# Kernel optimization log

Hardware: AMD Instinct MI355X
Metric: run time of the kernel (lower is better)

Reference implementation:

```python
import jax, jax.numpy as jnp
import numpy as np

DEGREE = 8
D = 512
K = 256
O = 512
N = 65536


def setup_inputs() -> dict:
    key = jax.random.key(0)
    ks = jax.random.split(key, 4)
    z = jax.random.normal(ks[0], (N, D), dtype=jnp.float32)
    T0 = jnp.ones((K,), dtype=jnp.float32)
    # T[i-1] corresponds to parameter T_i, i = 1..DEGREE, each [K, D]
    T = jax.random.normal(ks[1], (DEGREE, K, D), dtype=jnp.float32) * 0.02
    C_w = jax.random.normal(ks[2], (O, K), dtype=jnp.float32) * (1.0 / np.sqrt(K))
    C_b = jnp.zeros((O,), dtype=jnp.float32)
    return {"z": z, "T0": T0, "T": T, "C_w": C_w, "C_b": C_b}


def reference(z, T0, T, C_w, C_b):
    # z: [N, D]; T: [DEGREE, K, D]; recurrence over polynomial degree n:
    #   out_n = (z @ ((2n-1)/n * T_n).T) * out_{n-1} - (n-1)/n * out_{n-2}
    z = z.reshape(-1, D)
    out_prev2 = T0                                  # degree 0, [K] (broadcasts over N)
    out_prev1 = jnp.einsum('nd,kd->nk', z, T[0])    # degree 1, [N, K]
    for n in range(2, DEGREE + 1):
        a = (2.0 * n - 1.0) / n
        b = (n - 1.0) / n
        cur = jnp.einsum('nd,kd->nk', z, a * T[n - 1]) * out_prev1 - b * out_prev2
        out_prev2, out_prev1 = out_prev1, cur
    # layer_C applied to out_list[degree]
    return out_prev1 @ C_w.T + C_b
```

## Files before the change

kernel.cpp:

```cpp
#include <hip/hip_runtime.h>
#include <hip/hip_fp16.h>
#include <cstdint>

#define NROWS 65536
#define DIM   512
#define KDIM  256
#define ODIM  512
#define DEG   8
#define ZN    (NROWS * DIM)
#define TN    (DEG * KDIM * DIM)
#define CWN   (ODIM * KDIM)

typedef _Float16 f16x8 __attribute__((ext_vector_type(8)));
typedef float    f32x4 __attribute__((ext_vector_type(4)));


__device__ __forceinline__ void gld_lds16(const void* g, void* l) {
  __builtin_amdgcn_global_load_lds(
      (const __attribute__((address_space(1))) unsigned int*)g,
      (__attribute__((address_space(3))) unsigned int*)l, 16, 0, 0);
}

__device__ __forceinline__ unsigned pack2h(float a, float b) {
  union { _Float16 h[2]; unsigned u; } x;
  x.h[0] = (_Float16)a; x.h[1] = (_Float16)b;
  return x.u;
}

__device__ __forceinline__ int swz(int row, int chunk) {
  return (row << 7) | (((chunk + row) & 7) << 4);
}


__global__ void k_convert(const float* __restrict__ z,
                          const float* __restrict__ T,
                          const float* __restrict__ Cw,
                          _Float16* __restrict__ z16,
                          _Float16* __restrict__ Tb,
                          _Float16* __restrict__ Cwb) {
  long e = ((long)blockIdx.x * 256 + threadIdx.x) * 4;
  const float* src;
  _Float16* dst;
  float s = 1.0f;
  if (e < ZN) {
    src = z + e; dst = z16 + e;
  } else {
    long o = e - ZN;
    if (o < TN) {
      int n = (int)(o >> 17);
      s = (n == 0) ? 1.0f : (float)(2 * n + 1) / (float)(n + 1);
      src = T + o; dst = Tb + o;
    } else {
      long c = o - TN;
      if (c >= CWN) return;
      src = Cw + c; dst = Cwb + c;
    }
  }
  float4 v = *(const float4*)src;
  uint2 p; p.x = pack2h(v.x * s, v.y * s); p.y = pack2h(v.z * s, v.w * s);
  *(uint2*)dst = p;
}


__launch_bounds__(256, 3)
__global__ void k_poly(const _Float16* __restrict__ z16,
                       const float* __restrict__ T0,
                       const _Float16* __restrict__ Tb,
                       _Float16* __restrict__ u8) {
  __shared__ __align__(16) uint16_t As[128 * 64];
  __shared__ __align__(16) uint16_t Bs[2][128 * 64];

  const int tid = threadIdx.x;
  const int wave = tid >> 6, lane = tid & 63;

  const int id = blockIdx.x;
  const int super = id >> 8, rem = id & 255;
  const int kg = rem >> 4;
  const int rt = (super << 4) | (rem & 15);
  const int r0 = rt << 7;
  const int k0 = kg << 4;

  const int m_l = lane & 15, kq = lane >> 4;
  const int wrow = wave << 5;

  f32x4 acc[DEG][2];
#pragma unroll
  for (int n = 0; n < DEG; n++)
#pragma unroll
    for (int a = 0; a < 2; a++)
      acc[n][a] = (f32x4){0.f, 0.f, 0.f, 0.f};

  const _Float16* aptr[4];
  const _Float16* bptr[4];
  int lofs[4];
#pragma unroll
  for (int j = 0; j < 4; j++) {
    int lin = (j << 8) + tid;
    int row = lin >> 3;
    int c = ((lin & 7) - row) & 7;
    lofs[j] = lin << 4;
    aptr[j] = z16 + (size_t)(r0 + row) * DIM + (c << 3);
    int n = row >> 4, kk = row & 15;
    bptr[j] = Tb + (size_t)((n << 8) + k0 + kk) * DIM + (c << 3);
  }

#pragma unroll
  for (int j = 0; j < 4; j++) gld_lds16(bptr[j], (char*)Bs[0] + lofs[j]);
#pragma unroll
  for (int j = 0; j < 4; j++) bptr[j] += 64;

  for (int it = 0; it < DIM / 64; it++) {
    const int cur = it & 1;
    __builtin_amdgcn_sched_barrier(0);
    __builtin_amdgcn_s_barrier();
    __builtin_amdgcn_sched_barrier(0);

#pragma unroll
    for (int j = 0; j < 4; j++) gld_lds16(aptr[j], (char*)As + lofs[j]);
#pragma unroll
    for (int j = 0; j < 4; j++) aptr[j] += 64;

    if (it < DIM / 64 - 1) {
#pragma unroll
      for (int j = 0; j < 4; j++)
        gld_lds16(bptr[j], (char*)Bs[cur ^ 1] + lofs[j]);
#pragma unroll
      for (int j = 0; j < 4; j++) bptr[j] += 64;
      asm volatile("s_waitcnt vmcnt(4)" ::: "memory");
    } else {
      asm volatile("s_waitcnt vmcnt(0)" ::: "memory");
    }
    __builtin_amdgcn_sched_barrier(0);
    __builtin_amdgcn_s_barrier();
    __builtin_amdgcn_sched_barrier(0);

#pragma unroll
    for (int ks = 0; ks < 2; ks++) {
      const int chunk = (ks << 2) + kq;
      f16x8 af[2];
#pragma unroll
      for (int mf = 0; mf < 2; mf++)
        af[mf] = *(const f16x8*)((char*)As + swz(wrow + (mf << 4) + m_l, chunk));
#pragma unroll
      for (int n = 0; n < DEG; n++) {
        f16x8 bv = *(const f16x8*)((char*)Bs[cur] + swz((n << 4) + m_l, chunk));
#pragma unroll
        for (int mf = 0; mf < 2; mf++)
          acc[n][mf] = __builtin_amdgcn_mfma_f32_16x16x32_f16(
              af[mf], bv, acc[n][mf], 0, 0, 0);
      }
    }
  }

  const float bcoef[7] = {1.f/2.f, 2.f/3.f, 3.f/4.f, 4.f/5.f,
                          5.f/6.f, 6.f/7.f, 7.f/8.f};
  const int col = k0 + m_l;
  const float t0v = T0[col];
#pragma unroll
  for (int mf = 0; mf < 2; mf++) {
    f32x4 up2 = {t0v, t0v, t0v, t0v};
    f32x4 up1 = acc[0][mf];
#pragma unroll
    for (int n = 2; n <= DEG; n++) {
      f32x4 cur = acc[n - 1][mf] * up1 - bcoef[n - 2] * up2;
      up2 = up1; up1 = cur;
    }
    const int rbase = r0 + wrow + (mf << 4) + (kq << 2);
#pragma unroll
    for (int r = 0; r < 4; r++)
      u8[(size_t)(rbase + r) * KDIM + col] = (_Float16)up1[r];
  }
}


__launch_bounds__(256, 4)
__global__ void k_out(const _Float16* __restrict__ u8,
                      const _Float16* __restrict__ Cwb,
                      const float* __restrict__ Cb,
                      float* __restrict__ out) {
  __shared__ __align__(16) uint16_t As[2][128 * 64];
  __shared__ __align__(16) uint16_t Bs[64 * 64];

  const int tid = threadIdx.x;
  const int wave = tid >> 6, lane = tid & 63;

  const int id = blockIdx.x;
  const int xcd = id & 7;
  const int s = id >> 3;
  const int cg = s & 7;
  const int rt = (xcd << 6) | (s >> 3);
  const int r0 = rt << 7;
  const int c0 = cg << 6;

  const int m_l = lane & 15, kq = lane >> 4;
  const int wrow = wave << 5;

  f32x4 acc[2][4];
#pragma unroll
  for (int a = 0; a < 2; a++)
#pragma unroll
    for (int b = 0; b < 4; b++)
      acc[a][b] = (f32x4){0.f, 0.f, 0.f, 0.f};

  const _Float16* aptr[4];
  const _Float16* bptr[2];
  int lofsA[4], lofsB[2];
#pragma unroll
  for (int j = 0; j < 4; j++) {
    int lin = (j << 8) + tid;
    int row = lin >> 3;
    int c = ((lin & 7) - row) & 7;
    lofsA[j] = lin << 4;
    aptr[j] = u8 + (size_t)(r0 + row) * KDIM + (c << 3);
  }
#pragma unroll
  for (int j = 0; j < 2; j++) {
    int lin = (j << 8) + tid;
    int row = lin >> 3;
    int c = ((lin & 7) - row) & 7;
    lofsB[j] = lin << 4;
    bptr[j] = Cwb + (size_t)(c0 + row) * KDIM + (c << 3);
  }

#pragma unroll
  for (int j = 0; j < 4; j++) gld_lds16(aptr[j], (char*)As[0] + lofsA[j]);
#pragma unroll
  for (int j = 0; j < 4; j++) aptr[j] += 64;

  for (int it = 0; it < KDIM / 64; it++) {
    const int cur = it & 1;
    __builtin_amdgcn_sched_barrier(0);
    __builtin_amdgcn_s_barrier();
    __builtin_amdgcn_sched_barrier(0);

#pragma unroll
    for (int j = 0; j < 2; j++) gld_lds16(bptr[j], (char*)Bs + lofsB[j]);
#pragma unroll
    for (int j = 0; j < 2; j++) bptr[j] += 64;

    if (it < KDIM / 64 - 1) {
#pragma unroll
      for (int j = 0; j < 4; j++)
        gld_lds16(aptr[j], (char*)As[cur ^ 1] + lofsA[j]);
#pragma unroll
      for (int j = 0; j < 4; j++) aptr[j] += 64;
      asm volatile("s_waitcnt vmcnt(4)" ::: "memory");
    } else {
      asm volatile("s_waitcnt vmcnt(0)" ::: "memory");
    }
    __builtin_amdgcn_sched_barrier(0);
    __builtin_amdgcn_s_barrier();
    __builtin_amdgcn_sched_barrier(0);

#pragma unroll
    for (int ks = 0; ks < 2; ks++) {
      const int chunk = (ks << 2) + kq;
      f16x8 af[2];
#pragma unroll
      for (int mf = 0; mf < 2; mf++)
        af[mf] = *(const f16x8*)((char*)As[cur] + swz(wrow + (mf << 4) + m_l, chunk));
#pragma unroll
      for (int kf = 0; kf < 4; kf++) {
        f16x8 bv = *(const f16x8*)((char*)Bs + swz((kf << 4) + m_l, chunk));
#pragma unroll
        for (int mf = 0; mf < 2; mf++)
          acc[mf][kf] = __builtin_amdgcn_mfma_f32_16x16x32_f16(
              af[mf], bv, acc[mf][kf], 0, 0, 0);
      }
    }
  }

#pragma unroll
  for (int kf = 0; kf < 4; kf++) {
    const int col = c0 + (kf << 4) + m_l;
    const float cb = Cb[col];
#pragma unroll
    for (int mf = 0; mf < 2; mf++) {
      const int rbase = r0 + wrow + (mf << 4) + (kq << 2);
#pragma unroll
      for (int r = 0; r < 4; r++)
        out[(size_t)(rbase + r) * ODIM + col] = acc[mf][kf][r] + cb;
    }
  }
}


extern "C" void kernel_launch(void* const* d_in, const int* in_sizes, int n_in,
                              void* d_out, int out_size, void* d_ws, size_t ws_size,
                              hipStream_t stream) {
  const float* z  = (const float*)d_in[0];
  const float* T0 = (const float*)d_in[1];
  const float* T  = (const float*)d_in[2];
  const float* Cw = (const float*)d_in[3];
  const float* Cb = (const float*)d_in[4];
  float* out = (float*)d_out;

  char* ws = (char*)d_ws;
  _Float16* z16 = (_Float16*)ws;
  _Float16* Tb  = (_Float16*)(ws + (size_t)ZN * 2);
  _Float16* Cwb = (_Float16*)(ws + (size_t)ZN * 2 + (size_t)TN * 2);
  _Float16* u8  = (_Float16*)(ws + (size_t)ZN * 2 + (size_t)TN * 2 + (size_t)CWN * 2);

  k_convert<<<33920, 256, 0, stream>>>(z, T, Cw, z16, Tb, Cwb);
  k_poly<<<8192, 256, 0, stream>>>(z16, T0, Tb, u8);
  k_out<<<4096, 256, 0, stream>>>(u8, Cwb, Cb, out);
}
```

Baseline: 377.7 us.

## Register-prefetch A tiles in poly GEMM, double-buffer B in output GEMM, widen convert

The poly kernel now loads z tiles into registers two stages ahead and stores them to LDS itself, instead of issuing direct global-to-LDS loads that had to complete within the same iteration. This hides global latency behind the MFMA work. The output GEMM now double-buffers the C_w tile and prefetches both operands one stage ahead, lowering its occupancy hint from 4 to 3 blocks. The convert kernel handles 8 elements per thread with half the grid. The costs are extra registers and LDS, plus lower occupancy in k_out.

```diff
diff --git a/kernel.cpp b/kernel.cpp
--- a/kernel.cpp
+++ b/kernel.cpp
@@ -38,7 +38,7 @@
                           _Float16* __restrict__ z16,
                           _Float16* __restrict__ Tb,
                           _Float16* __restrict__ Cwb) {
-  long e = ((long)blockIdx.x * 256 + threadIdx.x) * 4;
+  long e = ((long)blockIdx.x * 256 + threadIdx.x) * 8;
   const float* src;
   _Float16* dst;
   float s = 1.0f;
@@ -56,9 +56,12 @@
       src = Cw + c; dst = Cwb + c;
     }
   }
-  float4 v = *(const float4*)src;
-  uint2 p; p.x = pack2h(v.x * s, v.y * s); p.y = pack2h(v.z * s, v.w * s);
-  *(uint2*)dst = p;
+  float4 v0 = *(const float4*)src;
+  float4 v1 = *(const float4*)(src + 4);
+  uint4 p;
+  p.x = pack2h(v0.x * s, v0.y * s); p.y = pack2h(v0.z * s, v0.w * s);
+  p.z = pack2h(v1.x * s, v1.y * s); p.w = pack2h(v1.z * s, v1.w * s);
+  *(uint4*)dst = p;
 }
 
 
@@ -104,32 +107,50 @@
     bptr[j] = Tb + (size_t)((n << 8) + k0 + kk) * DIM + (c << 3);
   }
 
+  uint4 aR[2][4];
+
+#pragma unroll
+  for (int j = 0; j < 4; j++)
+    aR[0][j] = *reinterpret_cast<const uint4*>(aptr[j]);
+  __builtin_amdgcn_sched_barrier(0);
 #pragma unroll
   for (int j = 0; j < 4; j++) gld_lds16(bptr[j], (char*)Bs[0] + lofs[j]);
-#pragma unroll
-  for (int j = 0; j < 4; j++) bptr[j] += 64;
-
+  __builtin_amdgcn_sched_barrier(0);
+#pragma unroll
+  for (int j = 0; j < 4; j++)
+    aR[1][j] = *reinterpret_cast<const uint4*>(aptr[j] + 64);
+  __builtin_amdgcn_sched_barrier(0);
+
+#pragma unroll
   for (int it = 0; it < DIM / 64; it++) {
     const int cur = it & 1;
-    __builtin_amdgcn_sched_barrier(0);
     __builtin_amdgcn_s_barrier();
-    __builtin_amdgcn_sched_barrier(0);
-
-#pragma unroll
-    for (int j = 0; j < 4; j++) gld_lds16(aptr[j], (char*)As + lofs[j]);
-#pragma unroll
-    for (int j = 0; j < 4; j++) aptr[j] += 64;
-
-    if (it < DIM / 64 - 1) {
+    if (it < DIM / 64 - 1)
+      asm volatile("s_waitcnt vmcnt(4)" ::: "memory");
+    else
+      asm volatile("s_waitcnt vmcnt(0)" ::: "memory");
+    __builtin_amdgcn_sched_barrier(0);
+
+#pragma unroll
+    for (int j = 0; j < 4; j++)
+      *(uint4*)((char*)As + lofs[j]) = aR[cur][j];
+    __builtin_amdgcn_sched_barrier(0);
+
+    if (it + 1 < DIM / 64) {
 #pragma unroll
       for (int j = 0; j < 4; j++)
-        gld_lds16(bptr[j], (char*)Bs[cur ^ 1] + lofs[j]);
-#pragma unroll
-      for (int j = 0; j < 4; j++) bptr[j] += 64;
-      asm volatile("s_waitcnt vmcnt(4)" ::: "memory");
-    } else {
-      asm volatile("s_waitcnt vmcnt(0)" ::: "memory");
-    }
+        gld_lds16(bptr[j] + ((it + 1) << 6), (char*)Bs[cur ^ 1] + lofs[j]);
+    }
+    __builtin_amdgcn_sched_barrier(0);
+
+    if (it + 2 < DIM / 64) {
+#pragma unroll
+      for (int j = 0; j < 4; j++)
+        aR[cur][j] = *reinterpret_cast<const uint4*>(aptr[j] + ((it + 2) << 6));
+    }
+    __builtin_amdgcn_sched_barrier(0);
+
+    asm volatile("s_waitcnt lgkmcnt(0)" ::: "memory");
     __builtin_amdgcn_sched_barrier(0);
     __builtin_amdgcn_s_barrier();
     __builtin_amdgcn_sched_barrier(0);
@@ -173,13 +194,13 @@
 }
 
 
-__launch_bounds__(256, 4)
+__launch_bounds__(256, 3)
 __global__ void k_out(const _Float16* __restrict__ u8,
                       const _Float16* __restrict__ Cwb,
                       const float* __restrict__ Cb,
                       float* __restrict__ out) {
   __shared__ __align__(16) uint16_t As[2][128 * 64];
-  __shared__ __align__(16) uint16_t Bs[64 * 64];
+  __shared__ __align__(16) uint16_t Bs[2][64 * 64];
 
   const int tid = threadIdx.x;
   const int wave = tid >> 6, lane = tid & 63;
@@ -224,27 +245,27 @@
 
 #pragma unroll
   for (int j = 0; j < 4; j++) gld_lds16(aptr[j], (char*)As[0] + lofsA[j]);
-#pragma unroll
-  for (int j = 0; j < 4; j++) aptr[j] += 64;
-
+  __builtin_amdgcn_sched_barrier(0);
+#pragma unroll
+  for (int j = 0; j < 2; j++) gld_lds16(bptr[j], (char*)Bs[0] + lofsB[j]);
+  __builtin_amdgcn_sched_barrier(0);
+
+#pragma unroll
   for (int it = 0; it < KDIM / 64; it++) {
     const int cur = it & 1;
-    __builtin_amdgcn_sched_barrier(0);
     __builtin_amdgcn_s_barrier();
     __builtin_amdgcn_sched_barrier(0);
 
-#pragma unroll
-    for (int j = 0; j < 2; j++) gld_lds16(bptr[j], (char*)Bs + lofsB[j]);
-#pragma unroll
-    for (int j = 0; j < 2; j++) bptr[j] += 64;
-
-    if (it < KDIM / 64 - 1) {
+    if (it + 1 < KDIM / 64) {
 #pragma unroll
       for (int j = 0; j < 4; j++)
-        gld_lds16(aptr[j], (char*)As[cur ^ 1] + lofsA[j]);
-#pragma unroll
-      for (int j = 0; j < 4; j++) aptr[j] += 64;
-      asm volatile("s_waitcnt vmcnt(4)" ::: "memory");
+        gld_lds16(aptr[j] + ((it + 1) << 6), (char*)As[cur ^ 1] + lofsA[j]);
+      __builtin_amdgcn_sched_barrier(0);
+#pragma unroll
+      for (int j = 0; j < 2; j++)
+        gld_lds16(bptr[j] + ((it + 1) << 6), (char*)Bs[cur ^ 1] + lofsB[j]);
+      __builtin_amdgcn_sched_barrier(0);
+      asm volatile("s_waitcnt vmcnt(6)" ::: "memory");
     } else {
       asm volatile("s_waitcnt vmcnt(0)" ::: "memory");
     }
@@ -261,7 +282,7 @@
         af[mf] = *(const f16x8*)((char*)As[cur] + swz(wrow + (mf << 4) + m_l, chunk));
 #pragma unroll
       for (int kf = 0; kf < 4; kf++) {
-        f16x8 bv = *(const f16x8*)((char*)Bs + swz((kf << 4) + m_l, chunk));
+        f16x8 bv = *(const f16x8*)((char*)Bs[cur] + swz((kf << 4) + m_l, chunk));
 #pragma unroll
         for (int mf = 0; mf < 2; mf++)
           acc[mf][kf] = __builtin_amdgcn_mfma_f32_16x16x32_f16(
@@ -301,7 +322,7 @@
   _Float16* Cwb = (_Float16*)(ws + (size_t)ZN * 2 + (size_t)TN * 2);
   _Float16* u8  = (_Float16*)(ws + (size_t)ZN * 2 + (size_t)TN * 2 + (size_t)CWN * 2);
 
-  k_convert<<<33920, 256, 0, stream>>>(z, T, Cw, z16, Tb, Cwb);
+  k_convert<<<16960, 256, 0, stream>>>(z, T, Cw, z16, Tb, Cwb);
   k_poly<<<8192, 256, 0, stream>>>(z16, T0, Tb, u8);
   k_out<<<4096, 256, 0, stream>>>(u8, Cwb, Cb, out);
 }
```

Result: slower. 394.3 us (+4.4%).
